# Kernel optimization log

Measured on AMD Instinct MI355X. Metric: run time of the kernel, lower is better.

## Reference

```python
import jax, jax.numpy as jnp
import numpy as np

EPS = 1e-5
NUM_HEADS = 8


def _ln(x, w, b):
    m = x.mean(-1, keepdims=True)
    v = jnp.mean(jnp.square(x - m), -1, keepdims=True)
    return (x - m) * jax.lax.rsqrt(v + EPS) * w + b


def _bn(x, w, b, mean, var):  # x: [N, C, T], eval-mode BatchNorm1d
    return (x - mean[None, :, None]) * jax.lax.rsqrt(var[None, :, None] + EPS) * w[None, :, None] + b[None, :, None]


def setup_inputs() -> dict:
    key = jax.random.key(0)
    ks = jax.random.split(key, 32)
    B, T, E, C = 8, 64, 128, 256
    H = 2 * C       # temporal conv hidden
    M = 4 * C       # mlp hidden
    s = 0.02
    f32 = jnp.float32
    inp = {
        'x': jax.random.normal(ks[0], (B, T, E, C), f32),
        'adj_mask': jax.random.randint(ks[1], (E, E), 0, 2, jnp.int32),
        'n1_w': 1.0 + s * jax.random.normal(ks[2], (C,), f32),
        'n1_b': s * jax.random.normal(ks[3], (C,), f32),
        'q_w': s * jax.random.normal(ks[4], (C, C), f32),
        'k_w': s * jax.random.normal(ks[5], (C, C), f32),
        'v_w': s * jax.random.normal(ks[6], (C, C), f32),
        'proj_w': s * jax.random.normal(ks[7], (C, C), f32),
        'proj_b': s * jax.random.normal(ks[8], (C,), f32),
        'on_w': 1.0 + s * jax.random.normal(ks[9], (C,), f32),
        'on_b': s * jax.random.normal(ks[10], (C,), f32),
        'gamma_s': jnp.asarray([0.5], f32),
        'conv1_w': s * jax.random.normal(ks[11], (H, C, 3), f32),
        'bn1_w': 1.0 + s * jax.random.normal(ks[12], (H,), f32),
        'bn1_b': s * jax.random.normal(ks[13], (H,), f32),
        'bn1_m': s * jax.random.normal(ks[14], (H,), f32),
        'bn1_v': jax.random.uniform(ks[15], (H,), f32, 0.5, 1.5),
        'conv2_w': s * jax.random.normal(ks[16], (C, H, 1), f32),
        'bn2_w': 1.0 + s * jax.random.normal(ks[17], (C,), f32),
        'bn2_b': s * jax.random.normal(ks[18], (C,), f32),
        'bn2_m': s * jax.random.normal(ks[19], (C,), f32),
        'bn2_v': jax.random.uniform(ks[20], (C,), f32, 0.5, 1.5),
        'tn_w': 1.0 + s * jax.random.normal(ks[21], (C,), f32),
        'tn_b': s * jax.random.normal(ks[22], (C,), f32),
        'gamma_t': jnp.asarray([0.5], f32),
        'n3_w': 1.0 + s * jax.random.normal(ks[23], (C,), f32),
        'n3_b': s * jax.random.normal(ks[24], (C,), f32),
        'fc1_w': s * jax.random.normal(ks[25], (C, M), f32),
        'fc1_b': s * jax.random.normal(ks[26], (M,), f32),
        'fc2_w': s * jax.random.normal(ks[27], (M, C), f32),
        'fc2_b': s * jax.random.normal(ks[28], (C,), f32),
    }
    return inp


def reference(x, adj_mask, n1_w, n1_b, q_w, k_w, v_w, proj_w, proj_b, on_w, on_b,
              gamma_s, conv1_w, bn1_w, bn1_b, bn1_m, bn1_v, conv2_w, bn2_w, bn2_b,
              bn2_m, bn2_v, tn_w, tn_b, gamma_t, n3_w, n3_b, fc1_w, fc1_b, fc2_w, fc2_b):
    B, T, E, C = x.shape
    Hh = NUM_HEADS
    D = C // Hh
    mask = adj_mask.astype(x.dtype)

    # ---- spatial geometric-cosine attention (per frame) ----
    xs = _ln(x, n1_w, n1_b)                                   # norm1
    q = (xs @ q_w).reshape(B, T, E, Hh, D)
    k = (xs @ k_w).reshape(B, T, E, Hh, D)
    v = (xs @ v_w).reshape(B, T, E, Hh, D)
    attn = jnp.einsum('btehd,btfhd->bthef', q, k)             # [B,T,H,E,E]
    attn = (attn * mask[None, None, None] + 1.0) * 0.5        # affine mask, no softmax
    o = jnp.einsum('bthef,btfhd->btehd', attn, v).reshape(B, T, E, C)
    o = _ln(o @ proj_w + proj_b, on_w, on_b)                  # proj + output_norm
    x = x + (xs + gamma_s * o)                                # inner + outer residual

    # ---- temporal convolution (norm2 is Identity) ----
    xt = _ln(x, tn_w, tn_b)
    xc = xt.transpose(0, 2, 3, 1).reshape(B * E, C, T)        # 'b t e c -> (b e) c t'
    dn = ('NCH', 'OIH', 'NCH')
    y = jax.lax.conv_general_dilated(xc, conv1_w, (1,), [(1, 1)], dimension_numbers=dn)
    y = jax.nn.gelu(_bn(y, bn1_w, bn1_b, bn1_m, bn1_v), approximate=False)
    y = jax.lax.conv_general_dilated(y, conv2_w, (1,), [(0, 0)], dimension_numbers=dn)
    y = _bn(y, bn2_w, bn2_b, bn2_m, bn2_v)
    y = y.reshape(B, E, C, T).transpose(0, 3, 1, 2)           # '(b e) c t -> b t e c'
    x = x + (x + gamma_t * y)                                 # temporal inner + outer residual

    # ---- MLP ----
    xm = _ln(x, n3_w, n3_b)
    h = jax.nn.gelu(xm @ fc1_w + fc1_b, approximate=False)
    x = x + (h @ fc2_w + fc2_b)
    return x
```

## Files before the change

### kernel.cpp

```cpp
#include <hip/hip_runtime.h>
#include <cstdint>

constexpr int Bn = 8, Tn = 64, En = 128, Cn = 256;
constexpr int Hn = 512, Mn = 1024, NHd = 8, Dn = 32;
constexpr int NTOK = Bn * Tn * En;
constexpr size_t SZ = (size_t)NTOK * Cn;
#define EPSF 1e-5f

typedef __attribute__((ext_vector_type(8))) short short8;
typedef __attribute__((ext_vector_type(4))) float f32x4;

__device__ __forceinline__ float bf2f(unsigned short u) {
  union { unsigned int i; float f; } c; c.i = ((unsigned int)u) << 16; return c.f;
}
__device__ __forceinline__ unsigned short f2bf(float f) {
  union { float f; unsigned int i; } c; c.f = f;
  unsigned int u = c.i;
  return (unsigned short)((u + 0x7fffu + ((u >> 16) & 1u)) >> 16);
}
__device__ __forceinline__ float gelu_f(float v) {
  float x2 = v * v;
  float p = v * fmaf(x2, 0.10294532f, 2.30221000f);
  float d = 1.0f + __builtin_amdgcn_exp2f(-p);
  return v * __builtin_amdgcn_rcpf(d);
}

__device__ __forceinline__ void gload16(const unsigned short* g, unsigned short* l) {
  __builtin_amdgcn_global_load_lds(
      (const __attribute__((address_space(1))) unsigned int*)g,
      (__attribute__((address_space(3))) unsigned int*)l, 16, 0, 0);
}

#define MEMFENCE() asm volatile("" ::: "memory")

template <int EPI, bool C1A, int KT, int NT>
__global__ __launch_bounds__(512) void mfma_gemm(
    const unsigned short* __restrict__ A,
    const unsigned short* __restrict__ Bt,
    const float* __restrict__ scale,
    const float* __restrict__ bias,
    const float* __restrict__ resf,
    const float* __restrict__ gscal,
    void* __restrict__ outv) {
  __shared__ unsigned short lds[4][2][8192];
  int tid = threadIdx.x;
  int lane = tid & 63, wave = tid >> 6;
  int wr = wave >> 2, wc = wave & 3;

  int nwg = gridDim.x * gridDim.y;
  int flat = blockIdx.y * gridDim.x + blockIdx.x;
  int cpx = nwg >> 3;
  int swz = (flat & 7) * cpx + (flat >> 3);
  int ntile = swz % gridDim.x;
  int mtile = swz / gridDim.x;
  int rowBase = mtile * 256;
  int colBase = ntile * 256;
  constexpr int lda = C1A ? 256 : KT;

  int arow = lane & 15, g8 = (lane >> 4) * 8;
  int aoff[8], boff[4];
#pragma unroll
  for (int m = 0; m < 8; ++m) aoff[m] = (wr * 128 + m * 16 + arow) * 32 + g8;
#pragma unroll
  for (int n = 0; n < 4; ++n) boff[n] = (wc * 64 + n * 16 + arow) * 32 + g8;

  f32x4 acc[8][4];
#pragma unroll
  for (int m = 0; m < 8; ++m)
#pragma unroll
    for (int n = 0; n < 4; ++n) acc[m][n] = (f32x4)(0.0f);

  int srow = lane >> 2;
  int scol = (lane & 3) * 8;

  auto stageA = [&](int T) {
    int k0 = T << 5, slot = T & 3;
#pragma unroll
    for (int r = 0; r < 2; ++r) {
      int row = r * 128 + wave * 16 + srow;
      const unsigned short* src;
      if (C1A) {
        int idx = rowBase + row;
        int bb = idx >> 13, tt = (idx >> 7) & 63, e = idx & 127;
        src = A + ((size_t)((bb * 66 + tt + (k0 >> 8)) * 128 + e)) * 256 +
              (k0 & 255) + scol;
      } else {
        src = A + (size_t)(rowBase + row) * lda + k0 + scol;
      }
      gload16(src, &lds[slot][0][r * 4096 + wave * 512]);
    }
  };
  auto stageB = [&](int T) {
    int k0 = T << 5, slot = T & 3;
#pragma unroll
    for (int r = 0; r < 2; ++r) {
      int row = r * 128 + wave * 16 + srow;
      const unsigned short* src = Bt + (size_t)(colBase + row) * KT + k0 + scol;
      gload16(src, &lds[slot][1][r * 4096 + wave * 512]);
    }
  };

  auto tile = [&](int T, int vm, bool st) {
    if (vm == 8)      asm volatile("s_waitcnt vmcnt(8)" ::: "memory");
    else if (vm == 4) asm volatile("s_waitcnt vmcnt(4)" ::: "memory");
    else              asm volatile("s_waitcnt vmcnt(0)" ::: "memory");
    __builtin_amdgcn_sched_barrier(0);
    __builtin_amdgcn_s_barrier();
    MEMFENCE();
    if (st) stageA(T + 3);
    const unsigned short* as = &lds[T & 3][0][0];
    const unsigned short* bs = &lds[T & 3][1][0];
    short8 bfr[4], af[4];
#pragma unroll
    for (int n = 0; n < 4; ++n) bfr[n] = *(const short8*)(bs + boff[n]);
#pragma unroll
    for (int m = 0; m < 4; ++m) af[m] = *(const short8*)(as + aoff[m]);
    __builtin_amdgcn_s_setprio(1);
#pragma unroll
    for (int m = 0; m < 4; ++m)
#pragma unroll
      for (int n = 0; n < 4; ++n)
        acc[m][n] = __builtin_amdgcn_mfma_f32_16x16x32_bf16(bfr[n], af[m], acc[m][n], 0, 0, 0);
    __builtin_amdgcn_s_setprio(0);
    if (st) stageB(T + 3);
#pragma unroll
    for (int m = 0; m < 4; ++m) af[m] = *(const short8*)(as + aoff[4 + m]);
    __builtin_amdgcn_s_setprio(1);
#pragma unroll
    for (int m = 0; m < 4; ++m)
#pragma unroll
      for (int n = 0; n < 4; ++n)
        acc[4 + m][n] = __builtin_amdgcn_mfma_f32_16x16x32_bf16(bfr[n], af[m], acc[4 + m][n], 0, 0, 0);
    __builtin_amdgcn_s_setprio(0);
  };

  stageA(0); stageB(0); stageA(1); stageB(1); stageA(2); stageB(2);
  constexpr int nkt = KT >> 5;
#pragma clang loop unroll(disable)
  for (int T = 0; T < nkt - 3; ++T) tile(T, 8, true);
  tile(nkt - 3, 8, false);
  tile(nkt - 2, 4, false);
  tile(nkt - 1, 0, false);
  MEMFENCE();

  int cm = lane & 15;
  int cn0 = (lane >> 4) * 4;
  size_t rb = (size_t)rowBase + wr * 128;
  int cb = colBase + wc * 64;
  float gt = (EPI == 3) ? gscal[0] : 0.f;
  float4 bi4[4], sc4[4];
#pragma unroll
  for (int n = 0; n < 4; ++n) {
    int col = cb + n * 16 + cn0;
    if (EPI != 0) bi4[n] = *(const float4*)(bias + col);
    if (EPI == 2 || EPI == 3) {
      if (scale) sc4[n] = *(const float4*)(scale + col);
      else { sc4[n].x = 1.f; sc4[n].y = 1.f; sc4[n].z = 1.f; sc4[n].w = 1.f; }
    }
  }
#pragma unroll
  for (int m = 0; m < 8; ++m) {
    size_t rowoff = (rb + m * 16 + cm) * (size_t)NT;
#pragma unroll
    for (int n = 0; n < 4; ++n) {
      int col = cb + n * 16 + cn0;
      f32x4 v = acc[m][n];
      if (EPI == 0) {
        ushort4 o = { f2bf(v[0]), f2bf(v[1]), f2bf(v[2]), f2bf(v[3]) };
        *(ushort4*)((unsigned short*)outv + rowoff + col) = o;
      } else if (EPI == 1) {
        ushort4 o = { f2bf(v[0] + bi4[n].x), f2bf(v[1] + bi4[n].y),
                      f2bf(v[2] + bi4[n].z), f2bf(v[3] + bi4[n].w) };
        *(ushort4*)((unsigned short*)outv + rowoff + col) = o;
      } else if (EPI == 2) {
        ushort4 o = { f2bf(gelu_f(v[0] * sc4[n].x + bi4[n].x)),
                      f2bf(gelu_f(v[1] * sc4[n].y + bi4[n].y)),
                      f2bf(gelu_f(v[2] * sc4[n].z + bi4[n].z)),
                      f2bf(gelu_f(v[3] * sc4[n].w + bi4[n].w)) };
        *(ushort4*)((unsigned short*)outv + rowoff + col) = o;
      } else if (EPI == 3) {
        float4 rf = *(const float4*)(resf + rowoff + col);
        float4 o;
        o.x = 2.0f * rf.x + gt * (v[0] * sc4[n].x + bi4[n].x);
        o.y = 2.0f * rf.y + gt * (v[1] * sc4[n].y + bi4[n].y);
        o.z = 2.0f * rf.z + gt * (v[2] * sc4[n].z + bi4[n].z);
        o.w = 2.0f * rf.w + gt * (v[3] * sc4[n].w + bi4[n].w);
        *(float4*)((float*)outv + rowoff + col) = o;
      } else if (EPI == 4) {
        float4 rf = *(const float4*)(resf + rowoff + col);
        float4 o;
        o.x = rf.x + v[0] + bi4[n].x;
        o.y = rf.y + v[1] + bi4[n].y;
        o.z = rf.z + v[2] + bi4[n].z;
        o.w = rf.w + v[3] + bi4[n].w;
        *(float4*)((float*)outv + rowoff + col) = o;
      } else if (EPI == 5) {
        float4 o;
        o.x = v[0] + bi4[n].x;
        o.y = v[1] + bi4[n].y;
        o.z = v[2] + bi4[n].z;
        o.w = v[3] + bi4[n].w;
        *(float4*)((float*)outv + rowoff + col) = o;
      }
    }
  }
}

template <bool PAD>
__global__ __launch_bounds__(256) void ln256_bf(const float* __restrict__ src,
                                                const float* __restrict__ w,
                                                const float* __restrict__ b,
                                                unsigned short* __restrict__ dst) {
  int lane = threadIdx.x & 63;
  int tok = blockIdx.x * 4 + (threadIdx.x >> 6);
  const float4* row = (const float4*)(src + (size_t)tok * Cn);
  float4 v = row[lane];
  float s  = v.x + v.y + v.z + v.w;
  float s2 = v.x*v.x + v.y*v.y + v.z*v.z + v.w*v.w;
#pragma unroll
  for (int off = 32; off >= 1; off >>= 1) {
    s  += __shfl_xor(s, off, 64);
    s2 += __shfl_xor(s2, off, 64);
  }
  float mean = s * (1.0f / Cn);
  float var = fmaxf(s2 * (1.0f / Cn) - mean * mean, 0.0f);
  float r = rsqrtf(var + EPSF);
  float4 wv = ((const float4*)w)[lane];
  float4 bv = ((const float4*)b)[lane];
  size_t dtok = tok;
  if (PAD) {
    int bb = tok >> 13, tt = (tok >> 7) & 63, e = tok & 127;
    dtok = ((size_t)(bb * 66 + tt + 1)) * 128 + e;
  }
  ushort4 o;
  o.x = f2bf((v.x - mean) * r * wv.x + bv.x);
  o.y = f2bf((v.y - mean) * r * wv.y + bv.y);
  o.z = f2bf((v.z - mean) * r * wv.z + bv.z);
  o.w = f2bf((v.w - mean) * r * wv.w + bv.w);
  *(ushort4*)(dst + dtok * Cn + lane * 4) = o;
}

__global__ __launch_bounds__(256) void ln_resid(const float* __restrict__ pjo,
                                                const float* __restrict__ w,
                                                const float* __restrict__ b,
                                                const float* __restrict__ x,
                                                const unsigned short* __restrict__ xs,
                                                const float* __restrict__ gs,
                                                float* __restrict__ x1) {
  int lane = threadIdx.x & 63;
  int tok = blockIdx.x * 4 + (threadIdx.x >> 6);
  size_t base = (size_t)tok * Cn;
  float4 v = ((const float4*)(pjo + base))[lane];
  float s  = v.x + v.y + v.z + v.w;
  float s2 = v.x*v.x + v.y*v.y + v.z*v.z + v.w*v.w;
#pragma unroll
  for (int off = 32; off >= 1; off >>= 1) {
    s  += __shfl_xor(s, off, 64);
    s2 += __shfl_xor(s2, off, 64);
  }
  float mean = s * (1.0f / Cn);
  float var = fmaxf(s2 * (1.0f / Cn) - mean * mean, 0.0f);
  float r = rsqrtf(var + EPSF);
  float4 wv = ((const float4*)w)[lane];
  float4 bv = ((const float4*)b)[lane];
  float g = gs[0];
  float4 xv = ((const float4*)(x + base))[lane];
  ushort4 s4 = ((const ushort4*)(xs + base))[lane];
  float4 o;
  o.x = xv.x + bf2f(s4.x) + g * ((v.x - mean) * r * wv.x + bv.x);
  o.y = xv.y + bf2f(s4.y) + g * ((v.y - mean) * r * wv.y + bv.y);
  o.z = xv.z + bf2f(s4.z) + g * ((v.z - mean) * r * wv.z + bv.z);
  o.w = xv.w + bf2f(s4.w) + g * ((v.w - mean) * r * wv.w + bv.w);
  ((float4*)(x1 + base))[lane] = o;
}

__global__ __launch_bounds__(256) void attn_mfma(const unsigned short* __restrict__ qkv,
                                                 const float* __restrict__ maskh,
                                                 unsigned short* __restrict__ o) {
  __shared__ unsigned short Qs[128 * 32];
  __shared__ unsigned short Ks[128 * 32];
  __shared__ unsigned short Vt[32 * 136];
  __shared__ unsigned short Ps[128 * 136];
  int tid = threadIdx.x, lane = tid & 63, wave = tid >> 6;
  int h = blockIdx.x & 7, bt = blockIdx.x >> 3;
  size_t gbase = (size_t)bt * 128 * 768 + h * 32;
#pragma unroll
  for (int i = 0; i < 2; ++i) {
    int q = wave * 2 + i;
    int row = q * 16 + (lane >> 2);
    int seg = (lane & 3) * 8;
    gload16(qkv + gbase + (size_t)row * 768 + seg, &Qs[q * 512]);
    gload16(qkv + gbase + 256 + (size_t)row * 768 + seg, &Ks[q * 512]);
  }
  {
    int e = tid >> 1, dh = (tid & 1) * 16;
    const unsigned short* gv = qkv + gbase + 512 + (size_t)e * 768 + dh;
    short8 v0 = *(const short8*)gv;
    short8 v1 = *(const short8*)(gv + 8);
#pragma unroll
    for (int j = 0; j < 8; ++j) {
      Vt[(dh + j) * 136 + e]     = (unsigned short)v0[j];
      Vt[(dh + 8 + j) * 136 + e] = (unsigned short)v1[j];
    }
  }
  __syncthreads();
  int arow = lane & 15, akk = (lane >> 4) * 8;
  int crow0 = (lane >> 4) * 4, ccol = lane & 15;
  short8 af0 = *(const short8*)&Qs[(wave * 32 + arow) * 32 + akk];
  short8 af1 = *(const short8*)&Qs[(wave * 32 + 16 + arow) * 32 + akk];
#pragma unroll
  for (int j = 0; j < 8; ++j) {
    short8 bfr = *(const short8*)&Ks[(j * 16 + arow) * 32 + akk];
    f32x4 s0 = __builtin_amdgcn_mfma_f32_16x16x32_bf16(af0, bfr, (f32x4)(0.0f), 0, 0, 0);
    f32x4 s1 = __builtin_amdgcn_mfma_f32_16x16x32_bf16(af1, bfr, (f32x4)(0.0f), 0, 0, 0);
    int f = j * 16 + ccol;
#pragma unroll
    for (int r = 0; r < 4; ++r) {
      int e0 = wave * 32 + crow0 + r;
      int e1 = e0 + 16;
      Ps[e0 * 136 + f] = f2bf(maskh[e0 * 128 + f] * s0[r] + 0.5f);
      Ps[e1 * 136 + f] = f2bf(maskh[e1 * 128 + f] * s1[r] + 0.5f);
    }
  }
  f32x4 acc[2][2];
#pragma unroll
  for (int i = 0; i < 2; ++i)
#pragma unroll
    for (int j = 0; j < 2; ++j) acc[i][j] = (f32x4)(0.0f);
#pragma unroll
  for (int k0 = 0; k0 < 128; k0 += 32) {
    short8 a0 = *(const short8*)&Ps[(wave * 32 + arow) * 136 + k0 + akk];
    short8 a1 = *(const short8*)&Ps[(wave * 32 + 16 + arow) * 136 + k0 + akk];
    short8 b0 = *(const short8*)&Vt[arow * 136 + k0 + akk];
    short8 b1 = *(const short8*)&Vt[(16 + arow) * 136 + k0 + akk];
    acc[0][0] = __builtin_amdgcn_mfma_f32_16x16x32_bf16(a0, b0, acc[0][0], 0, 0, 0);
    acc[0][1] = __builtin_amdgcn_mfma_f32_16x16x32_bf16(a0, b1, acc[0][1], 0, 0, 0);
    acc[1][0] = __builtin_amdgcn_mfma_f32_16x16x32_bf16(a1, b0, acc[1][0], 0, 0, 0);
    acc[1][1] = __builtin_amdgcn_mfma_f32_16x16x32_bf16(a1, b1, acc[1][1], 0, 0, 0);
  }
  unsigned short* ob = o + (size_t)bt * 128 * 256 + h * 32;
#pragma unroll
  for (int i = 0; i < 2; ++i)
#pragma unroll
    for (int j = 0; j < 2; ++j)
#pragma unroll
      for (int r = 0; r < 4; ++r) {
        int e = wave * 32 + i * 16 + crow0 + r;
        ob[(size_t)e * 256 + j * 16 + ccol] = f2bf(acc[i][j][r]);
      }
}

__global__ __launch_bounds__(256) void transcast(const float* __restrict__ src,
                                                 unsigned short* __restrict__ dst,
                                                 int N, int K) {
  int idx = blockIdx.x * 256 + threadIdx.x;
  int n = idx / K, k = idx - n * K;
  dst[idx] = f2bf(src[(size_t)k * N + n]);
}
__global__ __launch_bounds__(256) void castbf(const float* __restrict__ s,
                                              unsigned short* __restrict__ d) {
  int i = blockIdx.x * 256 + threadIdx.x;
  d[i] = f2bf(s[i]);
}
__global__ __launch_bounds__(256) void pack_conv1(const float* __restrict__ w1,
                                                  unsigned short* __restrict__ dst) {
  int idx = blockIdx.x * 256 + threadIdx.x;
  int hh = idx / 768, kk = idx - hh * 768;
  int slab = kk >> 8, c = kk & 255;
  dst[idx] = f2bf(w1[(size_t)hh * 768 + c * 3 + slab]);
}
__global__ __launch_bounds__(256) void bnfold(const float* __restrict__ w,
                                              const float* __restrict__ bvec,
                                              const float* __restrict__ m,
                                              const float* __restrict__ v,
                                              float* __restrict__ s,
                                              float* __restrict__ o, int n) {
  int i = blockIdx.x * 256 + threadIdx.x;
  if (i < n) {
    float sc = w[i] * rsqrtf(v[i] + EPSF);
    s[i] = sc;
    o[i] = bvec[i] - m[i] * sc;
  }
}
__global__ __launch_bounds__(256) void mask_prep(const int* __restrict__ adj,
                                                 float* __restrict__ maskh) {
  int i = blockIdx.x * 256 + threadIdx.x;
  maskh[i] = 0.5f * (float)adj[i];
}
__global__ __launch_bounds__(256) void zero_pad(unsigned short* __restrict__ xt) {
  int idx = blockIdx.x * 256 + threadIdx.x;
  int bb = idx >> 16;
  int rem = idx & 65535;
  int which = rem >> 15;
  int off = rem & 32767;
  size_t base = ((size_t)(bb * 66 + which * 65)) * 128 * 256;
  xt[base + off] = 0;
}

extern "C" void kernel_launch(void* const* d_in, const int* in_sizes, int n_in,
                              void* d_out, int out_size, void* d_ws, size_t ws_size,
                              hipStream_t stream) {
  (void)in_sizes; (void)n_in; (void)out_size; (void)ws_size;
  const float* x       = (const float*)d_in[0];
  const int*   adj     = (const int*)  d_in[1];
  const float* n1_w    = (const float*)d_in[2];
  const float* n1_b    = (const float*)d_in[3];
  const float* q_w     = (const float*)d_in[4];
  const float* k_w     = (const float*)d_in[5];
  const float* v_w     = (const float*)d_in[6];
  const float* proj_w  = (const float*)d_in[7];
  const float* proj_b  = (const float*)d_in[8];
  const float* on_w    = (const float*)d_in[9];
  const float* on_b    = (const float*)d_in[10];
  const float* gamma_s = (const float*)d_in[11];
  const float* conv1_w = (const float*)d_in[12];
  const float* bn1_w   = (const float*)d_in[13];
  const float* bn1_b   = (const float*)d_in[14];
  const float* bn1_m   = (const float*)d_in[15];
  const float* bn1_v   = (const float*)d_in[16];
  const float* conv2_w = (const float*)d_in[17];
  const float* bn2_w   = (const float*)d_in[18];
  const float* bn2_b   = (const float*)d_in[19];
  const float* bn2_m   = (const float*)d_in[20];
  const float* bn2_v   = (const float*)d_in[21];
  const float* tn_w    = (const float*)d_in[22];
  const float* tn_b    = (const float*)d_in[23];
  const float* gamma_t = (const float*)d_in[24];
  const float* n3_w    = (const float*)d_in[25];
  const float* n3_b    = (const float*)d_in[26];
  const float* fc1_w   = (const float*)d_in[27];
  const float* fc1_b   = (const float*)d_in[28];
  const float* fc2_w   = (const float*)d_in[29];
  const float* fc2_b   = (const float*)d_in[30];
  float* O = (float*)d_out;

  const size_t MB = 1024 * 1024;
  char* wsb = (char*)d_ws;
  unsigned short* qkvb = (unsigned short*)(wsb + 0);
  float*          pjo  = (float*)(wsb + 0);
  float*          x1b  = (float*)(wsb + 0);
  unsigned short* xmb  = (unsigned short*)(wsb + 0);
  unsigned short* hb   = (unsigned short*)(wsb + 32 * MB);
  unsigned short* xtp  = (unsigned short*)(wsb + 64 * MB);
  unsigned short* xsb  = (unsigned short*)(wsb + 96 * MB);
  unsigned short* oat  = (unsigned short*)(wsb + 128 * MB);
  unsigned short* y1b  = (unsigned short*)(wsb + 100 * MB);
  char* wp = wsb + 164 * MB;
  unsigned short* Wqkv = (unsigned short*)wp;  wp += 768 * 256 * 2;
  unsigned short* PjT  = (unsigned short*)wp;  wp += 256 * 256 * 2;
  unsigned short* W1t  = (unsigned short*)wp;  wp += 512 * 768 * 2;
  unsigned short* W2t  = (unsigned short*)wp;  wp += 256 * 512 * 2;
  unsigned short* F1t  = (unsigned short*)wp;  wp += 1024 * 256 * 2;
  unsigned short* F2t  = (unsigned short*)wp;  wp += 256 * 1024 * 2;
  float* s1 = (float*)wp; wp += 512 * 4;
  float* o1 = (float*)wp; wp += 512 * 4;
  float* s2 = (float*)wp; wp += 256 * 4;
  float* o2 = (float*)wp; wp += 256 * 4;
  float* maskh = (float*)wp; wp += 16384 * 4;

  transcast<<<768 * 256 / 256, 256, 0, stream>>>(q_w, Wqkv, 256, 256);
  transcast<<<768 * 256 / 256, 256, 0, stream>>>(k_w, Wqkv + 256 * 256, 256, 256);
  transcast<<<768 * 256 / 256, 256, 0, stream>>>(v_w, Wqkv + 512 * 256, 256, 256);
  transcast<<<256 * 256 / 256, 256, 0, stream>>>(proj_w, PjT, 256, 256);
  pack_conv1<<<512 * 768 / 256, 256, 0, stream>>>(conv1_w, W1t);
  castbf<<<256 * 512 / 256, 256, 0, stream>>>(conv2_w, W2t);
  transcast<<<1024 * 256 / 256, 256, 0, stream>>>(fc1_w, F1t, 1024, 256);
  transcast<<<256 * 1024 / 256, 256, 0, stream>>>(fc2_w, F2t, 256, 1024);
  bnfold<<<2, 256, 0, stream>>>(bn1_w, bn1_b, bn1_m, bn1_v, s1, o1, 512);
  bnfold<<<1, 256, 0, stream>>>(bn2_w, bn2_b, bn2_m, bn2_v, s2, o2, 256);
  mask_prep<<<64, 256, 0, stream>>>(adj, maskh);
  zero_pad<<<524288 / 256, 256, 0, stream>>>(xtp);

  ln256_bf<false><<<NTOK / 4, 256, 0, stream>>>(x, n1_w, n1_b, xsb);
  mfma_gemm<0, false, 256, 768><<<dim3(3, 256), 512, 0, stream>>>(xsb, Wqkv, nullptr, nullptr, nullptr, nullptr, qkvb);
  attn_mfma<<<Bn * Tn * NHd, 256, 0, stream>>>(qkvb, maskh, oat);
  mfma_gemm<5, false, 256, 256><<<dim3(1, 256), 512, 0, stream>>>(oat, PjT, nullptr, proj_b, nullptr, nullptr, pjo);
  ln_resid<<<NTOK / 4, 256, 0, stream>>>(pjo, on_w, on_b, x, xsb, gamma_s, x1b);

  ln256_bf<true><<<NTOK / 4, 256, 0, stream>>>(x1b, tn_w, tn_b, xtp);
  mfma_gemm<2, true, 768, 512><<<dim3(2, 256), 512, 0, stream>>>(xtp, W1t, s1, o1, nullptr, nullptr, y1b);
  mfma_gemm<3, false, 512, 256><<<dim3(1, 256), 512, 0, stream>>>(y1b, W2t, s2, o2, x1b, gamma_t, O);

  ln256_bf<false><<<NTOK / 4, 256, 0, stream>>>(O, n3_w, n3_b, xmb);
  mfma_gemm<2, false, 256, 1024><<<dim3(4, 256), 512, 0, stream>>>(xmb, F1t, nullptr, fc1_b, nullptr, nullptr, hb);
  mfma_gemm<4, false, 1024, 256><<<dim3(1, 256), 512, 0, stream>>>(hb, F2t, nullptr, fc2_b, O, nullptr, O);
}
```

Before: 615.1 us.

## Fuse MLP fc1+GELU and fc2 into one kernel keeping hidden chunk in LDS

Replaces the separate fc1 (with GELU) and fc2 GEMMs with a single kernel. Each block owns 256 rows and loops over 8 hidden chunks of 128. For each chunk it computes the fc1 tile, applies GELU, writes it to a swizzled LDS buffer, and immediately accumulates fc2 over that chunk. This removes the 64MB bf16 hidden activation round trip through global memory. In exchange it uses a large LDS footprint (~112KB), so occupancy is limited to one block per CU. It also launches only 256 blocks, and the xm tile is re-read from global/L2 for every chunk.

```diff
diff --git a/kernel.cpp b/kernel.cpp
--- a/kernel.cpp
+++ b/kernel.cpp
@@ -167,10 +167,6 @@
       f32x4 v = acc[m][n];
       if (EPI == 0) {
         ushort4 o = { f2bf(v[0]), f2bf(v[1]), f2bf(v[2]), f2bf(v[3]) };
-        *(ushort4*)((unsigned short*)outv + rowoff + col) = o;
-      } else if (EPI == 1) {
-        ushort4 o = { f2bf(v[0] + bi4[n].x), f2bf(v[1] + bi4[n].y),
-                      f2bf(v[2] + bi4[n].z), f2bf(v[3] + bi4[n].w) };
         *(ushort4*)((unsigned short*)outv + rowoff + col) = o;
       } else if (EPI == 2) {
         ushort4 o = { f2bf(gelu_f(v[0] * sc4[n].x + bi4[n].x)),
@@ -186,14 +182,6 @@
         o.z = 2.0f * rf.z + gt * (v[2] * sc4[n].z + bi4[n].z);
         o.w = 2.0f * rf.w + gt * (v[3] * sc4[n].w + bi4[n].w);
         *(float4*)((float*)outv + rowoff + col) = o;
-      } else if (EPI == 4) {
-        float4 rf = *(const float4*)(resf + rowoff + col);
-        float4 o;
-        o.x = rf.x + v[0] + bi4[n].x;
-        o.y = rf.y + v[1] + bi4[n].y;
-        o.z = rf.z + v[2] + bi4[n].z;
-        o.w = rf.w + v[3] + bi4[n].w;
-        *(float4*)((float*)outv + rowoff + col) = o;
       } else if (EPI == 5) {
         float4 o;
         o.x = v[0] + bi4[n].x;
@@ -202,6 +190,192 @@
         o.w = v[3] + bi4[n].w;
         *(float4*)((float*)outv + rowoff + col) = o;
       }
+    }
+  }
+}
+
+__global__ __launch_bounds__(512) void fused_mlp(
+    const unsigned short* __restrict__ xm,
+    const unsigned short* __restrict__ F1t,
+    const float* __restrict__ b1,
+    const unsigned short* __restrict__ F2t,
+    const float* __restrict__ b2,
+    float* __restrict__ O) {
+  __shared__ __align__(16) unsigned short g1A[2][8192];
+  __shared__ __align__(16) unsigned short g1B[2][4096];
+  __shared__ __align__(16) unsigned short g2B[2][8192];
+  __shared__ __align__(16) unsigned short hc[32768];
+  int tid = threadIdx.x, lane = tid & 63, wave = tid >> 6;
+  int wr = wave >> 2, wc = wave & 3;
+  size_t rowBase = (size_t)blockIdx.x * 256;
+  int arow = lane & 15, g8 = (lane >> 4) * 8;
+  int srow = lane >> 2, scol = (lane & 3) * 8;
+  int cm = lane & 15, cn0 = (lane >> 4) * 4;
+
+  f32x4 acc2[8][4];
+#pragma unroll
+  for (int m = 0; m < 8; ++m)
+#pragma unroll
+    for (int n = 0; n < 4; ++n) acc2[m][n] = (f32x4)(0.0f);
+
+  auto stage1A = [&](int t) {
+    int k0 = t << 5, slot = t & 1;
+#pragma unroll
+    for (int r = 0; r < 2; ++r) {
+      int row = r * 128 + wave * 16 + srow;
+      gload16(xm + (rowBase + row) * 256 + k0 + scol,
+              &g1A[slot][r * 4096 + wave * 512]);
+    }
+  };
+  auto stage1B = [&](int t, int c) {
+    int k0 = t << 5, slot = t & 1;
+    int row = wave * 16 + srow;
+    gload16(F1t + (size_t)(c * 128 + row) * 256 + k0 + scol,
+            &g1B[slot][wave * 512]);
+  };
+  auto stage2B = [&](int kk, int c) {
+    int slot = kk & 1;
+#pragma unroll
+    for (int r = 0; r < 2; ++r) {
+      int row = r * 128 + wave * 16 + srow;
+      gload16(F2t + (size_t)row * 1024 + c * 128 + kk * 32 + scol,
+              &g2B[slot][r * 4096 + wave * 512]);
+    }
+  };
+
+#pragma clang loop unroll(disable)
+  for (int c = 0; c < 8; ++c) {
+    f32x4 acc1[8][2];
+#pragma unroll
+    for (int m = 0; m < 8; ++m) { acc1[m][0] = (f32x4)(0.0f); acc1[m][1] = (f32x4)(0.0f); }
+    stage1A(0); stage1B(0, c);
+#pragma clang loop unroll(disable)
+    for (int t = 0; t < 8; ++t) {
+      __builtin_amdgcn_s_barrier();
+      MEMFENCE();
+      if (t < 7) {
+        stage1A(t + 1); stage1B(t + 1, c);
+        asm volatile("s_waitcnt vmcnt(3)" ::: "memory");
+      } else {
+        asm volatile("s_waitcnt vmcnt(0)" ::: "memory");
+      }
+      __builtin_amdgcn_sched_barrier(0);
+      __builtin_amdgcn_s_barrier();
+      MEMFENCE();
+      const unsigned short* as = &g1A[t & 1][0];
+      const unsigned short* bs = &g1B[t & 1][0];
+      short8 bf[2], af[4];
+#pragma unroll
+      for (int n = 0; n < 2; ++n)
+        bf[n] = *(const short8*)(bs + (wc * 32 + n * 16 + arow) * 32 + g8);
+#pragma unroll
+      for (int m = 0; m < 4; ++m)
+        af[m] = *(const short8*)(as + (wr * 128 + m * 16 + arow) * 32 + g8);
+      __builtin_amdgcn_s_setprio(1);
+#pragma unroll
+      for (int m = 0; m < 4; ++m)
+#pragma unroll
+        for (int n = 0; n < 2; ++n)
+          acc1[m][n] = __builtin_amdgcn_mfma_f32_16x16x32_bf16(bf[n], af[m], acc1[m][n], 0, 0, 0);
+      __builtin_amdgcn_s_setprio(0);
+#pragma unroll
+      for (int m = 0; m < 4; ++m)
+        af[m] = *(const short8*)(as + (wr * 128 + (4 + m) * 16 + arow) * 32 + g8);
+      __builtin_amdgcn_s_setprio(1);
+#pragma unroll
+      for (int m = 0; m < 4; ++m)
+#pragma unroll
+        for (int n = 0; n < 2; ++n)
+          acc1[4 + m][n] = __builtin_amdgcn_mfma_f32_16x16x32_bf16(bf[n], af[m], acc1[4 + m][n], 0, 0, 0);
+      __builtin_amdgcn_s_setprio(0);
+    }
+    float4 b1v[2];
+#pragma unroll
+    for (int n = 0; n < 2; ++n)
+      b1v[n] = *(const float4*)(b1 + c * 128 + wc * 32 + n * 16 + cn0);
+#pragma unroll
+    for (int m = 0; m < 8; ++m) {
+      int hrow = wr * 128 + m * 16 + cm;
+#pragma unroll
+      for (int n = 0; n < 2; ++n) {
+        int hcol = wc * 32 + n * 16 + cn0;
+        int eidx = (hrow * 128 + hcol) ^ ((hrow & 7) << 3);
+        float4 bv = b1v[n];
+        ushort4 hv = { f2bf(gelu_f(acc1[m][n][0] + bv.x)),
+                       f2bf(gelu_f(acc1[m][n][1] + bv.y)),
+                       f2bf(gelu_f(acc1[m][n][2] + bv.z)),
+                       f2bf(gelu_f(acc1[m][n][3] + bv.w)) };
+        *(ushort4*)&hc[eidx] = hv;
+      }
+    }
+    asm volatile("s_waitcnt lgkmcnt(0)" ::: "memory");
+    __builtin_amdgcn_sched_barrier(0);
+    __builtin_amdgcn_s_barrier();
+    MEMFENCE();
+    stage2B(0, c);
+#pragma clang loop unroll(disable)
+    for (int kk = 0; kk < 4; ++kk) {
+      __builtin_amdgcn_s_barrier();
+      MEMFENCE();
+      if (kk < 3) {
+        stage2B(kk + 1, c);
+        asm volatile("s_waitcnt vmcnt(2)" ::: "memory");
+      } else {
+        asm volatile("s_waitcnt vmcnt(0)" ::: "memory");
+      }
+      __builtin_amdgcn_sched_barrier(0);
+      __builtin_amdgcn_s_barrier();
+      MEMFENCE();
+      const unsigned short* bs = &g2B[kk & 1][0];
+      short8 bf2[4], af2[4];
+#pragma unroll
+      for (int n = 0; n < 4; ++n)
+        bf2[n] = *(const short8*)(bs + (wc * 64 + n * 16 + arow) * 32 + g8);
+#pragma unroll
+      for (int m = 0; m < 4; ++m) {
+        int row2 = wr * 128 + m * 16 + arow;
+        af2[m] = *(const short8*)&hc[(row2 * 128 + kk * 32 + g8) ^ ((row2 & 7) << 3)];
+      }
+      __builtin_amdgcn_s_setprio(1);
+#pragma unroll
+      for (int m = 0; m < 4; ++m)
+#pragma unroll
+        for (int n = 0; n < 4; ++n)
+          acc2[m][n] = __builtin_amdgcn_mfma_f32_16x16x32_bf16(bf2[n], af2[m], acc2[m][n], 0, 0, 0);
+      __builtin_amdgcn_s_setprio(0);
+#pragma unroll
+      for (int m = 0; m < 4; ++m) {
+        int row2 = wr * 128 + (4 + m) * 16 + arow;
+        af2[m] = *(const short8*)&hc[(row2 * 128 + kk * 32 + g8) ^ ((row2 & 7) << 3)];
+      }
+      __builtin_amdgcn_s_setprio(1);
+#pragma unroll
+      for (int m = 0; m < 4; ++m)
+#pragma unroll
+        for (int n = 0; n < 4; ++n)
+          acc2[4 + m][n] = __builtin_amdgcn_mfma_f32_16x16x32_bf16(bf2[n], af2[m], acc2[4 + m][n], 0, 0, 0);
+      __builtin_amdgcn_s_setprio(0);
+    }
+  }
+  MEMFENCE();
+  float4 b2v[4];
+#pragma unroll
+  for (int n = 0; n < 4; ++n)
+    b2v[n] = *(const float4*)(b2 + wc * 64 + n * 16 + cn0);
+#pragma unroll
+  for (int m = 0; m < 8; ++m) {
+    size_t rowoff = (rowBase + wr * 128 + m * 16 + cm) * 256;
+#pragma unroll
+    for (int n = 0; n < 4; ++n) {
+      int col = wc * 64 + n * 16 + cn0;
+      float4 rf = *(const float4*)(O + rowoff + col);
+      f32x4 v = acc2[m][n];
+      float4 o;
+      o.x = rf.x + v[0] + b2v[n].x;
+      o.y = rf.y + v[1] + b2v[n].y;
+      o.z = rf.z + v[2] + b2v[n].z;
+      o.w = rf.w + v[3] + b2v[n].w;
+      *(float4*)(O + rowoff + col) = o;
     }
   }
 }
@@ -440,7 +614,6 @@
   float*          pjo  = (float*)(wsb + 0);
   float*          x1b  = (float*)(wsb + 0);
   unsigned short* xmb  = (unsigned short*)(wsb + 0);
-  unsigned short* hb   = (unsigned short*)(wsb + 32 * MB);
   unsigned short* xtp  = (unsigned short*)(wsb + 64 * MB);
   unsigned short* xsb  = (unsigned short*)(wsb + 96 * MB);
   unsigned short* oat  = (unsigned short*)(wsb + 128 * MB);
@@ -482,6 +655,5 @@
   mfma_gemm<3, false, 512, 256><<<dim3(1, 256), 512, 0, stream>>>(y1b, W2t, s2, o2, x1b, gamma_t, O);
 
   ln256_bf<false><<<NTOK / 4, 256, 0, stream>>>(O, n3_w, n3_b, xmb);
-  mfma_gemm<2, false, 256, 1024><<<dim3(4, 256), 512, 0, stream>>>(xmb, F1t, nullptr, fc1_b, nullptr, nullptr, hb);
-  mfma_gemm<4, false, 1024, 256><<<dim3(1, 256), 512, 0, stream>>>(hb, F2t, nullptr, fc2_b, O, nullptr, O);
-}
+  fused_mlp<<<256, 512, 0, stream>>>(xmb, F1t, fc1_b, F2t, fc2_b, O);
+}
```

Measured after the change: 646.3 us. +5.1%, slower.
